# Optimization experiments

Hardware: AMD Instinct MI355X
Metric: run time of the kernel (lower is better)

## Reference

```python
import jax, jax.numpy as jnp
import numpy as np


def _knn_indices(x, k):
    # Brute-force exact kNN via squared-euclidean distances (matches sklearn
    # NearestNeighbors fit on x, queried with x: self is included as a neighbor).
    sq = jnp.sum(x * x, axis=1)                      # [N]
    d = sq[:, None] + sq[None, :] - 2.0 * (x @ x.T)  # [N, N] squared distances
    _, idx = jax.lax.top_k(-d, k)                    # k smallest distances
    return idx                                        # [N, k] int32


def setup_inputs() -> dict:
    key = jax.random.key(0)
    k1, k2 = jax.random.split(key)
    N, D = 10000, 128
    return {
        "input": jax.random.normal(k1, (N, D), dtype=jnp.float32),
        "target": jax.random.normal(k2, (N, D), dtype=jnp.float32),
        "k": 15,
    }


def reference(input, target, k):
    N = input.shape[0]
    in_idx = _knn_indices(input, k)    # [N, k]
    tgt_idx = _knn_indices(target, k)  # [N, k]
    # Per-row set intersection size: neighbor indices within a row are unique,
    # so counting pairwise equality matches np.intersect1d(...).shape[0].
    matches = in_idx[:, :, None] == tgt_idx[:, None, :]  # [N, k, k]
    overlap = jnp.sum(matches)
    loss = 1.0 - overlap.astype(jnp.float32) / jnp.float32(N * k)
    return loss
```

## Files before the change

### kernel.cpp

```cpp
#include <hip/hip_runtime.h>
#include <hip/hip_bf16.h>
#include <stdint.h>

#define NROW 10000
#define DIM 128
#define NP 10240
#define KSEL 15
#define JC 32
#define NTILES (NP / 16)
#define TPC (NTILES / JC)

typedef __attribute__((ext_vector_type(4))) float f32x4;
typedef __attribute__((ext_vector_type(8))) short s16x8;
using bf16_t = __hip_bfloat16;

#define GLD16(gsrc, ldst)                                                          \
    __builtin_amdgcn_global_load_lds(                                              \
        (const __attribute__((address_space(1))) void*)(gsrc),                     \
        (__attribute__((address_space(3))) void*)(ldst), 16, 0, 0)

__global__ __launch_bounds__(256)
void knn_convert(const float* __restrict__ x0, const float* __restrict__ x1,
                 bf16_t* __restrict__ xp, float* __restrict__ sqh,
                 unsigned* __restrict__ counter)
{
    if (blockIdx.x == 0 && threadIdx.x == 0) *counter = 0u;
    const int rg   = blockIdx.x * 4 + (threadIdx.x >> 6);
    const int lane = threadIdx.x & 63;
    if (rg >= 2 * NP) return;
    const int m = rg >= NP ? 1 : 0;
    const int r = rg - m * NP;
    const float* src = m ? x1 : x0;

    float2 v = make_float2(0.f, 0.f);
    float  s = 0.f;
    if (r < NROW) {
        v = *(const float2*)(src + (size_t)r * DIM + lane * 2);
        s = v.x * v.x + v.y * v.y;
    }
    const uint32_t pk = (uint32_t)__bfloat16_as_ushort(__float2bfloat16(v.x))
                      | ((uint32_t)__bfloat16_as_ushort(__float2bfloat16(v.y)) << 16);
    const int e   = lane * 2;
    const int kk  = e >> 5;
    const int gg  = (e >> 3) & 3;
    const int pos = e & 7;
    const size_t off = ((((size_t)m * NTILES + (r >> 4)) * 4 + kk) * 64
                        + (size_t)(gg * 16 + (r & 15))) * 8 + pos;
    *(uint32_t*)(xp + off) = pk;
    #pragma unroll
    for (int o = 32; o; o >>= 1) s += __shfl_down(s, o);
    if (lane == 0) sqh[m * NP + r] = (r < NROW) ? fmaf(s, -0.5f, 1024.0f) : 1.0f;
}

#define PACKMAX(acc, idxb, Q)                                                     \
    do {                                                                          \
        const uint32_t k0_ = (__float_as_uint((acc)[0]) & 0xFFFFFC00u) | (idxb);  \
        const uint32_t k1_ = (__float_as_uint((acc)[1]) & 0xFFFFFC00u) | ((idxb) | 1u); \
        const uint32_t k2_ = (__float_as_uint((acc)[2]) & 0xFFFFFC00u) | ((idxb) | 2u); \
        const uint32_t k3_ = (__float_as_uint((acc)[3]) & 0xFFFFFC00u) | ((idxb) | 3u); \
        asm("v_max3_u32 %0, %1, %2, %0" : "+v"(Q) : "v"(k0_), "v"(k1_));          \
        asm("v_max3_u32 %0, %1, %2, %0" : "+v"(Q) : "v"(k2_), "v"(k3_));          \
    } while (0)

#define MFMA4(d, set, cin)                                                        \
    f32x4 d = __builtin_amdgcn_mfma_f32_16x16x32_bf16(a0, bfr##set[0], cin, 0, 0, 0); \
    d = __builtin_amdgcn_mfma_f32_16x16x32_bf16(a1, bfr##set[1], d, 0, 0, 0);     \
    d = __builtin_amdgcn_mfma_f32_16x16x32_bf16(a2, bfr##set[2], d, 0, 0, 0);     \
    d = __builtin_amdgcn_mfma_f32_16x16x32_bf16(a3, bfr##set[3], d, 0, 0, 0)

__global__ __launch_bounds__(256, 3)
void knn_topk(const bf16_t* __restrict__ xp, const float* __restrict__ sqh,
              uint32_t* __restrict__ pk2, uint16_t* __restrict__ px2)
{
    __shared__ bf16_t Abuf[2][2048];
    __shared__ float  Sbuf[512];

    const int m     = blockIdx.z;
    const int chunk = blockIdx.y;
    const int ib    = blockIdx.x * 256;
    const int wave  = threadIdx.x >> 6;
    const int lane  = threadIdx.x & 63;
    const int li    = lane & 15;
    const int g     = lane >> 4;
    const int tid   = threadIdx.x;

    const bf16_t* XP = xp + (size_t)m * NP * DIM;
    const float*  SQ = sqh + m * NP;

    const int t0 = chunk * TPC;
    const bf16_t* XC = XP + (size_t)t0 * 2048;
    const float*  SC = SQ + t0 * 16;

    if (wave < 2)
        GLD16(SC + (size_t)(wave * 64 + lane) * 4, &Sbuf[wave * 256]);
    GLD16(XC + (size_t)tid * 8, &Abuf[0][wave * 512]);

    const int ti0 = (ib >> 4) + wave * 4;
    s16x8 bfr0[4], bfr1[4], bfr2[4], bfr3[4];
    #pragma unroll
    for (int kk = 0; kk < 4; ++kk) {
        const size_t bo = ((size_t)kk * 64 + (size_t)(g * 16 + li)) * 8;
        bfr0[kk] = *(const s16x8*)(XP + (size_t)ti0 * 2048 + bo);
        bfr1[kk] = *(const s16x8*)(XP + (size_t)(ti0 + 1) * 2048 + bo);
        bfr2[kk] = *(const s16x8*)(XP + (size_t)(ti0 + 2) * 2048 + bo);
        bfr3[kk] = *(const s16x8*)(XP + (size_t)(ti0 + 3) * 2048 + bo);
    }

    uint32_t q0 = 0, q1 = 0, q2 = 0, q3 = 0;

    const bf16_t* pf = XC + 2048 + (size_t)tid * 8;

    for (int t = 0; t < TPC; ++t) {
        __syncthreads();

        const bf16_t* ab = &Abuf[t & 1][lane * 8];
        const s16x8 a0 = *(const s16x8*)(ab);
        const s16x8 a1 = *(const s16x8*)(ab + 512);
        const s16x8 a2 = *(const s16x8*)(ab + 1024);
        const s16x8 a3 = *(const s16x8*)(ab + 1536);
        const f32x4 sv = *(const f32x4*)&Sbuf[t * 16 + g * 4];

        GLD16(pf, &Abuf[(t + 1) & 1][wave * 512]);
        pf += 2048;

        MFMA4(acc0, 0, sv);
        MFMA4(acc1, 1, sv);
        MFMA4(acc2, 2, sv);
        MFMA4(acc3, 3, sv);

        const uint32_t ib4 = (uint32_t)(t << 2);
        PACKMAX(acc0, ib4, q0);
        PACKMAX(acc1, ib4, q1);
        PACKMAX(acc2, ib4, q2);
        PACKMAX(acc3, ib4, q3);
    }

    const size_t base = ((size_t)((m * JC + chunk) * 4 + g)) * NP;
    #pragma unroll
    for (int s = 0; s < 4; ++s) {
        const uint32_t q = (s == 0) ? q0 : (s == 1) ? q1 : (s == 2) ? q2 : q3;
        const uint32_t id = q & 1023u;
        const int j = (t0 + (int)(id >> 2)) * 16 + g * 4 + (int)(id & 3u);
        const int i = ib + wave * 64 + s * 16 + li;
        pk2[base + i] = q;
        px2[base + i] = (uint16_t)j;
    }
}

#define INS(k, hi, lo) asm("v_med3_u32 %0, %1, %2, %0" : "+v"(lo) : "v"(k), "v"(hi))

__global__ __launch_bounds__(256, 1)
void knn_select_half(const uint32_t* __restrict__ pk2, const uint16_t* __restrict__ px2,
                     uint32_t* __restrict__ sk, uint16_t* __restrict__ sx)
{
    const int i = blockIdx.x * 256 + threadIdx.x;
    const int m = blockIdx.y;
    const int h = blockIdx.z;
    if (i >= NROW) return;

    const uint32_t* pv = pk2 + ((size_t)(m * 128 + h * 64)) * NP + i;
    const uint16_t* px = px2 + ((size_t)(m * 128 + h * 64)) * NP + i;

    uint32_t k[64]; uint16_t jx[64];
    #pragma unroll
    for (int c = 0; c < 64; ++c) {
        k[c]  = pv[(size_t)c * NP];
        jx[c] = px[(size_t)c * NP];
    }
    uint32_t q0 = 0, q1 = 0, q2 = 0, q3 = 0, q4 = 0, q5 = 0, q6 = 0, q7 = 0,
             q8 = 0, q9 = 0, q10 = 0, q11 = 0, q12 = 0, q13 = 0, q14 = 0;
    #pragma unroll
    for (int c = 0; c < 64; ++c) {
        const uint32_t kc = k[c];
        INS(kc, q13, q14); INS(kc, q12, q13); INS(kc, q11, q12); INS(kc, q10, q11);
        INS(kc, q9,  q10); INS(kc, q8,  q9);  INS(kc, q7,  q8);  INS(kc, q6,  q7);
        INS(kc, q5,  q6);  INS(kc, q4,  q5);  INS(kc, q3,  q4);  INS(kc, q2,  q3);
        INS(kc, q1,  q2);  INS(kc, q0,  q1);
        q0 = (q0 > kc) ? q0 : kc;
    }
    const uint32_t thr = q14;
    uint32_t* ok = sk + ((size_t)(m * 2 + h) * KSEL) * NROW + i;
    uint16_t* ox = sx + ((size_t)(m * 2 + h) * KSEL) * NROW + i;
    int n = 0;
    #pragma unroll
    for (int c = 0; c < 64; ++c) {
        if (k[c] >= thr && n < KSEL) {
            ok[(size_t)n * NROW] = k[c];
            ox[(size_t)n * NROW] = jx[c];
            n++;
        }
    }
}

__global__ __launch_bounds__(256, 1)
void knn_merge_count(const uint32_t* __restrict__ sk, const uint16_t* __restrict__ sx,
                     unsigned* __restrict__ counter)
{
    __shared__ uint16_t ids[256][KSEL + 3];
    __shared__ int wsum[4];
    const int tid  = blockIdx.x * 256 + threadIdx.x;
    const int m    = tid & 1;
    const int i    = tid >> 1;
    const int lane = threadIdx.x & 63;
    const int wave = threadIdx.x >> 6;

    if (i < NROW) {
        const uint32_t* pv = sk + (size_t)(m * 2 * KSEL) * NROW + i;
        const uint16_t* px = sx + (size_t)(m * 2 * KSEL) * NROW + i;
        uint32_t k[2 * KSEL]; uint16_t jx[2 * KSEL];
        #pragma unroll
        for (int c = 0; c < 2 * KSEL; ++c) {
            k[c]  = pv[(size_t)c * NROW];
            jx[c] = px[(size_t)c * NROW];
        }
        uint32_t q0 = 0, q1 = 0, q2 = 0, q3 = 0, q4 = 0, q5 = 0, q6 = 0, q7 = 0,
                 q8 = 0, q9 = 0, q10 = 0, q11 = 0, q12 = 0, q13 = 0, q14 = 0;
        #pragma unroll
        for (int c = 0; c < 2 * KSEL; ++c) {
            const uint32_t kc = k[c];
            INS(kc, q13, q14); INS(kc, q12, q13); INS(kc, q11, q12); INS(kc, q10, q11);
            INS(kc, q9,  q10); INS(kc, q8,  q9);  INS(kc, q7,  q8);  INS(kc, q6,  q7);
            INS(kc, q5,  q6);  INS(kc, q4,  q5);  INS(kc, q3,  q4);  INS(kc, q2,  q3);
            INS(kc, q1,  q2);  INS(kc, q0,  q1);
            q0 = (q0 > kc) ? q0 : kc;
        }
        const uint32_t thr = q14;
        int n = 0;
        #pragma unroll
        for (int c = 0; c < 2 * KSEL; ++c) {
            if (k[c] >= thr && n < KSEL) { ids[threadIdx.x][n] = jx[c]; n++; }
        }
    }
    __syncthreads();

    int cnt = 0;
    if (i < NROW && m == 0) {
        #pragma unroll
        for (int a = 0; a < KSEL; ++a) {
            const uint16_t x = ids[threadIdx.x][a];
            #pragma unroll
            for (int b = 0; b < KSEL; ++b)
                cnt += (x == ids[threadIdx.x + 1][b]) ? 1 : 0;
        }
    }
    #pragma unroll
    for (int off = 32; off; off >>= 1) cnt += __shfl_down(cnt, off);
    if (lane == 0) wsum[wave] = cnt;
    __syncthreads();
    if (threadIdx.x == 0)
        atomicAdd(counter, (unsigned)(wsum[0] + wsum[1] + wsum[2] + wsum[3]));
}

__global__ void knn_finalize(const unsigned* __restrict__ counter, float* __restrict__ out)
{
    out[0] = 1.0f - (float)(*counter) / (float)(NROW * KSEL);
}

#define XPAD (4 * 2048)
#define SQPAD 512

extern "C" void kernel_launch(void* const* d_in, const int* in_sizes, int n_in,
                              void* d_out, int out_size, void* d_ws, size_t ws_size,
                              hipStream_t stream)
{
    (void)in_sizes; (void)n_in; (void)out_size; (void)ws_size;
    const float* x0 = (const float*)d_in[0];
    const float* x1 = (const float*)d_in[1];
    float* out = (float*)d_out;

    char* ws = (char*)d_ws;
    size_t off = 0;
    bf16_t* xp  = (bf16_t*)(ws + off); off += ((size_t)2 * NP * DIM + XPAD) * sizeof(bf16_t);
    float*  sqh = (float*)(ws + off);  off += ((size_t)2 * NP + SQPAD) * sizeof(float);
    off = (off + 255) & ~(size_t)255;
    uint32_t* pk2 = (uint32_t*)(ws + off); off += (size_t)2 * JC * 4 * NP * sizeof(uint32_t);
    uint16_t* px2 = (uint16_t*)(ws + off); off += (size_t)2 * JC * 4 * NP * sizeof(uint16_t);
    off = (off + 255) & ~(size_t)255;
    uint32_t* sk = (uint32_t*)(ws + off); off += (size_t)4 * KSEL * NROW * sizeof(uint32_t);
    uint16_t* sx = (uint16_t*)(ws + off); off += (size_t)4 * KSEL * NROW * sizeof(uint16_t);
    off = (off + 255) & ~(size_t)255;
    unsigned* counter = (unsigned*)(ws + off);

    knn_convert<<<(2 * NP) / 4, 256, 0, stream>>>(x0, x1, xp, sqh, counter);
    knn_topk<<<dim3(NP / 256, JC, 2), 256, 0, stream>>>(xp, sqh, pk2, px2);
    knn_select_half<<<dim3((NROW + 255) / 256, 2, 2), 256, 0, stream>>>(pk2, px2, sk, sx);
    knn_merge_count<<<(2 * NROW + 255) / 256, 256, 0, stream>>>(sk, sx, counter);
    knn_finalize<<<1, 1, 0, stream>>>(counter, out);
}
```

Before: 72.02 us.

## Use 512-thread blocks with two tiles per wave and two A tiles per barrier

knn_topk now runs 8 waves per block instead of 4. Each wave keeps two resident B tiles instead of four, so it holds fewer registers. Each loop iteration stages two 16-row A tiles into a larger double buffer, which halves the number of barriers per chunk. The goal is more resident waves and less synchronisation, at the cost of more LDS reads of A per MFMA and a larger shared footprint. The final prefetch now reads two tiles past the chunk end, so it relies on enough workspace padding after the data.

```diff
diff --git a/kernel.cpp b/kernel.cpp
--- a/kernel.cpp
+++ b/kernel.cpp
@@ -68,11 +68,11 @@
     d = __builtin_amdgcn_mfma_f32_16x16x32_bf16(a2, bfr##set[2], d, 0, 0, 0);     \
     d = __builtin_amdgcn_mfma_f32_16x16x32_bf16(a3, bfr##set[3], d, 0, 0, 0)
 
-__global__ __launch_bounds__(256, 3)
+__global__ __launch_bounds__(512)
 void knn_topk(const bf16_t* __restrict__ xp, const float* __restrict__ sqh,
               uint32_t* __restrict__ pk2, uint16_t* __restrict__ px2)
 {
-    __shared__ bf16_t Abuf[2][2048];
+    __shared__ bf16_t Abuf[2][4096];
     __shared__ float  Sbuf[512];
 
     const int m     = blockIdx.z;
@@ -95,53 +95,60 @@
         GLD16(SC + (size_t)(wave * 64 + lane) * 4, &Sbuf[wave * 256]);
     GLD16(XC + (size_t)tid * 8, &Abuf[0][wave * 512]);
 
-    const int ti0 = (ib >> 4) + wave * 4;
-    s16x8 bfr0[4], bfr1[4], bfr2[4], bfr3[4];
+    const int ti0 = (ib >> 4) + wave * 2;
+    s16x8 bfr0[4], bfr1[4];
     #pragma unroll
     for (int kk = 0; kk < 4; ++kk) {
         const size_t bo = ((size_t)kk * 64 + (size_t)(g * 16 + li)) * 8;
         bfr0[kk] = *(const s16x8*)(XP + (size_t)ti0 * 2048 + bo);
         bfr1[kk] = *(const s16x8*)(XP + (size_t)(ti0 + 1) * 2048 + bo);
-        bfr2[kk] = *(const s16x8*)(XP + (size_t)(ti0 + 2) * 2048 + bo);
-        bfr3[kk] = *(const s16x8*)(XP + (size_t)(ti0 + 3) * 2048 + bo);
-    }
-
-    uint32_t q0 = 0, q1 = 0, q2 = 0, q3 = 0;
-
-    const bf16_t* pf = XC + 2048 + (size_t)tid * 8;
-
-    for (int t = 0; t < TPC; ++t) {
+    }
+
+    uint32_t q0 = 0, q1 = 0;
+
+    const bf16_t* pf = XC + 2 * 2048 + (size_t)tid * 8;
+
+    for (int p = 0; p < TPC / 2; ++p) {
         __syncthreads();
 
-        const bf16_t* ab = &Abuf[t & 1][lane * 8];
-        const s16x8 a0 = *(const s16x8*)(ab);
-        const s16x8 a1 = *(const s16x8*)(ab + 512);
-        const s16x8 a2 = *(const s16x8*)(ab + 1024);
-        const s16x8 a3 = *(const s16x8*)(ab + 1536);
-        const f32x4 sv = *(const f32x4*)&Sbuf[t * 16 + g * 4];
-
-        GLD16(pf, &Abuf[(t + 1) & 1][wave * 512]);
-        pf += 2048;
-
-        MFMA4(acc0, 0, sv);
-        MFMA4(acc1, 1, sv);
-        MFMA4(acc2, 2, sv);
-        MFMA4(acc3, 3, sv);
-
-        const uint32_t ib4 = (uint32_t)(t << 2);
-        PACKMAX(acc0, ib4, q0);
-        PACKMAX(acc1, ib4, q1);
-        PACKMAX(acc2, ib4, q2);
-        PACKMAX(acc3, ib4, q3);
+        GLD16(pf, &Abuf[(p + 1) & 1][wave * 512]);
+        pf += 4096;
+
+        const bf16_t* ab = &Abuf[p & 1][lane * 8];
+
+        {
+            const s16x8 a0 = *(const s16x8*)(ab);
+            const s16x8 a1 = *(const s16x8*)(ab + 512);
+            const s16x8 a2 = *(const s16x8*)(ab + 1024);
+            const s16x8 a3 = *(const s16x8*)(ab + 1536);
+            const f32x4 sv = *(const f32x4*)&Sbuf[(2 * p) * 16 + g * 4];
+            MFMA4(acc0, 0, sv);
+            MFMA4(acc1, 1, sv);
+            const uint32_t ib4 = (uint32_t)((2 * p) << 2);
+            PACKMAX(acc0, ib4, q0);
+            PACKMAX(acc1, ib4, q1);
+        }
+        {
+            const s16x8 a0 = *(const s16x8*)(ab + 2048);
+            const s16x8 a1 = *(const s16x8*)(ab + 2048 + 512);
+            const s16x8 a2 = *(const s16x8*)(ab + 2048 + 1024);
+            const s16x8 a3 = *(const s16x8*)(ab + 2048 + 1536);
+            const f32x4 sv = *(const f32x4*)&Sbuf[(2 * p + 1) * 16 + g * 4];
+            MFMA4(acc0, 0, sv);
+            MFMA4(acc1, 1, sv);
+            const uint32_t ib4 = (uint32_t)((2 * p + 1) << 2);
+            PACKMAX(acc0, ib4, q0);
+            PACKMAX(acc1, ib4, q1);
+        }
     }
 
     const size_t base = ((size_t)((m * JC + chunk) * 4 + g)) * NP;
     #pragma unroll
-    for (int s = 0; s < 4; ++s) {
-        const uint32_t q = (s == 0) ? q0 : (s == 1) ? q1 : (s == 2) ? q2 : q3;
+    for (int s = 0; s < 2; ++s) {
+        const uint32_t q = (s == 0) ? q0 : q1;
         const uint32_t id = q & 1023u;
         const int j = (t0 + (int)(id >> 2)) * 16 + g * 4 + (int)(id & 3u);
-        const int i = ib + wave * 64 + s * 16 + li;
+        const int i = ib + wave * 32 + s * 16 + li;
         pk2[base + i] = q;
         px2[base + i] = (uint16_t)j;
     }
@@ -282,7 +289,7 @@
     unsigned* counter = (unsigned*)(ws + off);
 
     knn_convert<<<(2 * NP) / 4, 256, 0, stream>>>(x0, x1, xp, sqh, counter);
-    knn_topk<<<dim3(NP / 256, JC, 2), 256, 0, stream>>>(xp, sqh, pk2, px2);
+    knn_topk<<<dim3(NP / 256, JC, 2), 512, 0, stream>>>(xp, sqh, pk2, px2);
     knn_select_half<<<dim3((NROW + 255) / 256, 2, 2), 256, 0, stream>>>(pk2, px2, sk, sx);
     knn_merge_count<<<(2 * NROW + 255) / 256, 256, 0, stream>>>(sk, sx, counter);
     knn_finalize<<<1, 1, 0, stream>>>(counter, out);
```

New measurement: 75.46 us. 4.8% more time.
